# Kernel optimization log

Measured on AMD Instinct MI355X. Metric: run time of the kernel, lower is better.

Reference implementation:

```python
import jax, jax.numpy as jnp
import numpy as np

NUM_FEATURES = 8
HIDDEN = 64
IN_DIM = NUM_FEATURES + 6  # 14


def _lstm_cell(x, h, c, W_ih, W_hh, b_ih, b_hh):
    # torch gate order: i, f, g, o
    gates = x @ W_ih.T + h @ W_hh.T + b_ih + b_hh
    i, f, g, o = jnp.split(gates, 4, axis=-1)
    c_new = jax.nn.sigmoid(f) * c + jax.nn.sigmoid(i) * jnp.tanh(g)
    h_new = jax.nn.sigmoid(o) * jnp.tanh(c_new)
    return h_new, c_new


def setup_inputs() -> dict:
    key = jax.random.key(0)
    ks = jax.random.split(key, 20)
    T = 20000
    s = 0.05
    inp = {
        "encoder_out": jax.random.normal(ks[0], (1024, 64), jnp.float32),
        "h0": jax.random.normal(ks[1], (2, HIDDEN), jnp.float32),
        "c0": jax.random.normal(ks[2], (2, HIDDEN), jnp.float32),
        "difficulty": jax.random.normal(ks[3], (6,), jnp.float32),
        "target": jax.random.normal(ks[4], (T, NUM_FEATURES), jnp.float32),
        # LSTM layer 0 (input 14 -> hidden 64)
        "W_ih0": jax.random.normal(ks[5], (4 * HIDDEN, IN_DIM), jnp.float32) * s,
        "W_hh0": jax.random.normal(ks[6], (4 * HIDDEN, HIDDEN), jnp.float32) * s,
        "b_ih0": jax.random.normal(ks[7], (4 * HIDDEN,), jnp.float32) * s,
        "b_hh0": jax.random.normal(ks[8], (4 * HIDDEN,), jnp.float32) * s,
        # LSTM layer 1 (hidden 64 -> hidden 64)
        "W_ih1": jax.random.normal(ks[9], (4 * HIDDEN, HIDDEN), jnp.float32) * s,
        "W_hh1": jax.random.normal(ks[10], (4 * HIDDEN, HIDDEN), jnp.float32) * s,
        "b_ih1": jax.random.normal(ks[11], (4 * HIDDEN,), jnp.float32) * s,
        "b_hh1": jax.random.normal(ks[12], (4 * HIDDEN,), jnp.float32) * s,
        # hiddenfc: 64 -> 32
        "W_hid": jax.random.normal(ks[13], (HIDDEN // 2, HIDDEN), jnp.float32) * s,
        "b_hid": jax.random.normal(ks[14], (HIDDEN // 2,), jnp.float32) * s,
        # outputfc: 32 -> 8
        "W_out": jax.random.normal(ks[15], (NUM_FEATURES, HIDDEN // 2), jnp.float32) * s,
        "b_out": jax.random.normal(ks[16], (NUM_FEATURES,), jnp.float32) * s,
    }
    return inp


def reference(encoder_out, h0, c0, difficulty, target,
              W_ih0, W_hh0, b_ih0, b_hh0,
              W_ih1, W_hh1, b_ih1, b_hh1,
              W_hid, b_hid, W_out, b_out):
    T = target.shape[0]
    # Teacher-forced inputs: step 0 is zeros(14); step i>0 is cat(target[i-1], difficulty).
    diff_tiled = jnp.broadcast_to(difficulty, (T - 1, 6))
    inputs = jnp.concatenate([
        jnp.zeros((1, IN_DIM), target.dtype),
        jnp.concatenate([target[:-1], diff_tiled], axis=1),
    ], axis=0)  # [T, 14]

    def step(carry, x_t):
        h0s, c0s, h1s, c1s = carry
        h0s, c0s = _lstm_cell(x_t, h0s, c0s, W_ih0, W_hh0, b_ih0, b_hh0)
        h1s, c1s = _lstm_cell(h0s, h1s, c1s, W_ih1, W_hh1, b_ih1, b_hh1)
        # dropout is identity in eval mode
        hid = h1s @ W_hid.T + b_hid
        out = jnp.round(hid @ W_out.T + b_out)
        return (h0s, c0s, h1s, c1s), out

    init = (h0[0], c0[0], h0[1], c0[1])
    (hf0, cf0, hf1, cf1), outs = jax.lax.scan(step, init, inputs)
    h_final = jnp.stack([hf0, hf1])  # [2, 64]
    c_final = jnp.stack([cf0, cf1])  # [2, 64]
    return outs, h_final, c_final
```

## Files before the change

### kernel.cpp

```cpp
#include <hip/hip_runtime.h>

#define NF 8
#define RD 256
#define RMASK 255

typedef float f2 __attribute__((ext_vector_type(2)));
typedef float f4 __attribute__((ext_vector_type(4)));

template <int CTRL>
__device__ __forceinline__ float qp(float x) {
  return __int_as_float(
      __builtin_amdgcn_update_dpp(0, __float_as_int(x), CTRL, 0xF, 0xF, true));
}

__device__ __forceinline__ void wg_barrier() {
  asm volatile("s_waitcnt lgkmcnt(0)" ::: "memory");
  __builtin_amdgcn_s_barrier();
  __builtin_amdgcn_sched_barrier(0);
}

__global__ __launch_bounds__(384, 2) void decoder_p10(
    const float* __restrict__ h0in, const float* __restrict__ c0in,
    const float* __restrict__ diffp, const float* __restrict__ target,
    const float* __restrict__ Wih0, const float* __restrict__ Whh0,
    const float* __restrict__ bih0, const float* __restrict__ bhh0,
    const float* __restrict__ Wih1, const float* __restrict__ Whh1,
    const float* __restrict__ bih1, const float* __restrict__ bhh1,
    const float* __restrict__ Whid, const float* __restrict__ bhidp,
    const float* __restrict__ Woutp, const float* __restrict__ boutp,
    float* __restrict__ outp, float* __restrict__ ws, const int T)
{
  const int tid = threadIdx.x;
  const int wv  = tid >> 6;
  const int l   = tid & 63;
  const int q   = l >> 2;
  const int k   = l & 3;
  const int u   = 16 * (wv & 3) + q;
  const int r   = 64 * k + u;
  const bool isk0 = (k == 0);
  const float am = (k == 2) ? 2.0f : 1.0f;
  const float ab = (k == 2) ? -1.0f : 0.0f;

  __shared__ alignas(256) float h0r[4][64];
  __shared__ alignas(256) float tbuf[2][32 * NF];
  __shared__ alignas(256) float h0loc[8][64];
  __shared__ alignas(256) float h1r[4][64];
  __shared__ alignas(256) float hidS[4][32];
  __shared__ alignas(256) float obuf[64 * NF];
  __shared__ float ldspad[23040];

  if (T < 0) {
    ldspad[tid] = h0in[tid];
    __syncthreads();
    outp[0] = ldspad[383 - tid];
  }

  int* flag = (int*)ws;
  int* cons = (int*)ws + 16;
  float* ring = ws + 64;

  if (blockIdx.x == 0) {
    f2 wreg[36];
    float b_ = 0.f, xd = 0.f, cS = 0.f, hS = 0.f, xc = 0.f;
    if (wv < 4) {
      #pragma unroll
      for (int j = 0; j < 4; ++j) {
        const int row = 64 * ((k + j) & 3) + u;
        const float* rp = Whh0 + row * 64 + 16 * k;
        #pragma unroll
        for (int c = 0; c < 4; ++c) {
          f4 v = *(const f4*)(rp + 4 * ((c + k) & 3));
          wreg[8 * j + 2 * c]     = v.lo;
          wreg[8 * j + 2 * c + 1] = v.hi;
        }
      }
      b_ = bih0[r] + bhh0[r];
      const float* ra = Wih0 + r * 14;
      #pragma unroll
      for (int c = 0; c < 4; ++c) wreg[32 + c] = (f2){ra[2 * c], ra[2 * c + 1]};
      #pragma unroll
      for (int m = 0; m < 6; ++m) xd += ra[8 + m] * diffp[m];
      if (isk0) cS = c0in[u];
      if (wv == 0) h0r[3][l] = h0in[l];
    } else if (wv == 5) {
      if (l < T) {
        *(f4*)&((float*)tbuf)[l * 8]     = *(const f4*)&target[l * 8];
        *(f4*)&((float*)tbuf)[l * 8 + 4] = *(const f4*)&target[l * 8 + 4];
      }
    }
    __syncthreads();

    int consL = 0;
    f4 tr0 = {0.f, 0.f, 0.f, 0.f}, tr1 = {0.f, 0.f, 0.f, 0.f};
    for (int t = 0; t <= T; ++t) {
      if (wv < 4) {
        if (t < T) {
          const float* base = &h0r[(t - 1) & 3][16 * k];
          f2 P0 = {0.f,0.f}, P1 = {0.f,0.f}, P2 = {0.f,0.f}, P3 = {0.f,0.f};
          #pragma unroll
          for (int c = 0; c < 4; ++c) {
            f4 v = *(const f4*)(base + 4 * ((c + k) & 3));
            P0 += wreg[2*c] * v.lo;      P0 += wreg[2*c+1] * v.hi;
            P1 += wreg[8+2*c] * v.lo;    P1 += wreg[8+2*c+1] * v.hi;
            P2 += wreg[16+2*c] * v.lo;   P2 += wreg[16+2*c+1] * v.hi;
            P3 += wreg[24+2*c] * v.lo;   P3 += wreg[24+2*c+1] * v.hi;
          }
          float p0 = P0.x + P0.y, p1 = P1.x + P1.y;
          float p2 = P2.x + P2.y, p3 = P3.x + P3.y;
          float g = ((p0 + qp<0x39>(p3)) + (qp<0x4E>(p2) + qp<0x93>(p1))) + b_ + xc;
          float e = __expf(-g * am);
          float s = __fdividef(1.0f, 1.0f + e);
          float a = fmaf(s, am, ab);
          float A1 = qp<0xB1>(a), A2 = qp<0x4E>(a), A3 = qp<0x1B>(a);
          if (isk0) {
            cS = A1 * cS + a * A2;
            float e2 = __expf(-2.0f * cS);
            hS = A3 * (__fdividef(2.0f, 1.0f + e2) - 1.0f);
            h0r[t & 3][u] = hS;
          }
        }
        if (t < T - 1) {
          const f4* trow = (const f4*)&tbuf[(t >> 5) & 1][(t & 31) * NF];
          f4 r0 = trow[0], r1 = trow[1];
          f2 s2 = wreg[32] * r0.lo; s2 += wreg[33] * r0.hi;
          s2 += wreg[34] * r1.lo;   s2 += wreg[35] * r1.hi;
          xc = xd + s2.x + s2.y;
        } else xc = 0.f;
      } else if (wv == 4) {
        if (t >= 1) {
          if ((t & 3) == 0 && t >= 4 && l == 0)
            __hip_atomic_store(flag, t - 2, __ATOMIC_RELEASE,
                               __HIP_MEMORY_SCOPE_AGENT);
          if ((t & 63) == 0) {
            while (t - consL > RD - 64)
              consL = __hip_atomic_load(cons, __ATOMIC_RELAXED,
                                        __HIP_MEMORY_SCOPE_AGENT);
          }
          ring[((t - 1) & RMASK) * 64 + l] = h0r[(t - 1) & 3][l];
        }
      } else {
        const int ph = t & 31;
        const int cl = (t >> 5) + 1;
        if (l < 32 && cl * 32 < T) {
          if (ph == 8) {
            tr0 = *(const f4*)&target[cl * 256 + l * 8];
            tr1 = *(const f4*)&target[cl * 256 + l * 8 + 4];
          } else if (ph == 26) {
            *(f4*)&tbuf[cl & 1][l * 8]     = tr0;
            *(f4*)&tbuf[cl & 1][l * 8 + 4] = tr1;
          }
        }
      }
      wg_barrier();
    }
    if (wv == 4 && l == 0)
      __hip_atomic_store(flag, T, __ATOMIC_RELEASE, __HIP_MEMORY_SCOPE_AGENT);
    if (wv < 4 && isk0) {
      outp[T * NF + u]       = hS;
      outp[T * NF + 128 + u] = cS;
    }
  } else {
    f2 wreg[64];
    f2 wH[16], wO[4];
    float b_ = 0.f, cS = 0.f, hS = 0.f;
    float bhA = 0.f, bhB = 0.f, bo_ = 0.f;
    if (wv < 4) {
      const float* Wsrc = (k < 2) ? Wih1 : Whh1;
      const int co = 32 * (k & 1);
      #pragma unroll
      for (int j = 0; j < 4; ++j) {
        const int row = 64 * ((k + j) & 3) + u;
        const float* rp = Wsrc + row * 64 + co;
        #pragma unroll
        for (int c = 0; c < 8; ++c) {
          f4 v = *(const f4*)(rp + 4 * ((c + 2 * k) & 7));
          wreg[16 * j + 2 * c]     = v.lo;
          wreg[16 * j + 2 * c + 1] = v.hi;
        }
      }
      b_ = bih1[r] + bhh1[r];
      if (isk0) cS = c0in[64 + u];
      if (wv == 0) h1r[3][l] = h0in[64 + l];
    } else if (wv == 5) {
      #pragma unroll
      for (int i = 0; i < 2; ++i) {
        const float* rp = Whid + (2 * q + i) * 64 + 16 * k;
        #pragma unroll
        for (int c = 0; c < 4; ++c) {
          f4 v = *(const f4*)(rp + 4 * ((c + k) & 3));
          wH[8 * i + 2 * c]     = v.lo;
          wH[8 * i + 2 * c + 1] = v.hi;
        }
      }
      bhA = bhidp[2 * q];
      bhB = bhidp[2 * q + 1];
      if (q < 8) {
        const float* rp = Woutp + q * 32 + 8 * k;
        #pragma unroll
        for (int c = 0; c < 2; ++c) {
          f4 v = *(const f4*)(rp + 4 * ((c + k) & 1));
          wO[2 * c]     = v.lo;
          wO[2 * c + 1] = v.hi;
        }
        bo_ = boutp[q];
      }
    }
    int flagL = 0, fillW = 0, nPend = 0;
    float b0 = 0.f, b1 = 0.f, b2 = 0.f, b3 = 0.f;
    if (wv == 4) {
      const int pre = (T < 4) ? T : 4;
      while (flagL < pre)
        flagL = __hip_atomic_load(flag, __ATOMIC_ACQUIRE,
                                  __HIP_MEMORY_SCOPE_AGENT);
      for (int s = 0; s < pre; ++s) {
        float v = ring[(s & RMASK) * 64 + l];
        h0loc[s & 7][l] = v;
      }
      fillW = pre;
    }
    __syncthreads();

    const int pend = T + 3;
    for (int p = 0; p <= pend; ++p) {
      if (wv < 4) {
        if (p < T) {
          const float* base = (k < 2) ? &h0loc[p & 7][32 * (k & 1)]
                                      : &h1r[(p - 1) & 3][32 * (k & 1)];
          f2 P0 = {0.f,0.f}, P1 = {0.f,0.f}, P2 = {0.f,0.f}, P3 = {0.f,0.f};
          #pragma unroll
          for (int c = 0; c < 8; ++c) {
            f4 v = *(const f4*)(base + 4 * ((c + 2 * k) & 7));
            P0 += wreg[2*c] * v.lo;      P0 += wreg[2*c+1] * v.hi;
            P1 += wreg[16+2*c] * v.lo;   P1 += wreg[16+2*c+1] * v.hi;
            P2 += wreg[32+2*c] * v.lo;   P2 += wreg[32+2*c+1] * v.hi;
            P3 += wreg[48+2*c] * v.lo;   P3 += wreg[48+2*c+1] * v.hi;
          }
          float p0 = P0.x + P0.y, p1 = P1.x + P1.y;
          float p2 = P2.x + P2.y, p3 = P3.x + P3.y;
          float g = ((p0 + qp<0x39>(p3)) + (qp<0x4E>(p2) + qp<0x93>(p1))) + b_;
          float e = __expf(-g * am);
          float s = __fdividef(1.0f, 1.0f + e);
          float a = fmaf(s, am, ab);
          float A1 = qp<0xB1>(a), A2 = qp<0x4E>(a), A3 = qp<0x1B>(a);
          if (isk0) {
            cS = A1 * cS + a * A2;
            float e2 = __expf(-2.0f * cS);
            hS = A3 * (__fdividef(2.0f, 1.0f + e2) - 1.0f);
            h1r[p & 3][u] = hS;
          }
        }
      } else if (wv == 4) {
        if (nPend > 0) h0loc[(fillW + 0) & 7][l] = b0;
        if (nPend > 1) h0loc[(fillW + 1) & 7][l] = b1;
        if (nPend > 2) h0loc[(fillW + 2) & 7][l] = b2;
        if (nPend > 3) h0loc[(fillW + 3) & 7][l] = b3;
        fillW += nPend;
        nPend = 0;
        if ((p & 3) == 0)
          flagL = __hip_atomic_load(flag, __ATOMIC_ACQUIRE,
                                    __HIP_MEMORY_SCOPE_AGENT);
        int need = p + 2; if (need > T) need = T;
        while (fillW < need) {
          while (flagL < fillW + 1)
            flagL = __hip_atomic_load(flag, __ATOMIC_ACQUIRE,
                                      __HIP_MEMORY_SCOPE_AGENT);
          float v = ring[(fillW & RMASK) * 64 + l];
          h0loc[fillW & 7][l] = v;
          ++fillW;
        }
        int want = flagL;
        if (want > p + 8) want = p + 8;
        if (want > T) want = T;
        int n = want - fillW;
        if (n < 0) n = 0;
        if (n > 4) n = 4;
        if (n > 0) b0 = ring[((fillW + 0) & RMASK) * 64 + l];
        if (n > 1) b1 = ring[((fillW + 1) & RMASK) * 64 + l];
        if (n > 2) b2 = ring[((fillW + 2) & RMASK) * 64 + l];
        if (n > 3) b3 = ring[((fillW + 3) & RMASK) * 64 + l];
        nPend = n;
        if ((p & 63) == 0 && l == 0)
          __hip_atomic_store(cons, p, __ATOMIC_RELAXED,
                             __HIP_MEMORY_SCOPE_AGENT);
      } else {
        const int sH = p - 2;
        if (sH >= 0 && sH < T) {
          const float* hp = &h1r[sH & 3][16 * k];
          f2 pa = {0.f,0.f}, pb = {0.f,0.f};
          #pragma unroll
          for (int c = 0; c < 4; ++c) {
            f4 v = *(const f4*)(hp + 4 * ((c + k) & 3));
            pa += wH[2*c] * v.lo;     pa += wH[2*c+1] * v.hi;
            pb += wH[8+2*c] * v.lo;   pb += wH[8+2*c+1] * v.hi;
          }
          float sa = pa.x + pa.y; sa += qp<0xB1>(sa); sa += qp<0x4E>(sa);
          float sb = pb.x + pb.y; sb += qp<0xB1>(sb); sb += qp<0x4E>(sb);
          if (isk0) *(f2*)&hidS[sH & 3][2 * q] = (f2){sa + bhA, sb + bhB};
        }
        const int sO = p - 4;
        if (sO >= 0 && sO < T && q < 8) {
          const float* hp = &hidS[sO & 3][8 * k];
          f2 po = {0.f,0.f};
          #pragma unroll
          for (int c = 0; c < 2; ++c) {
            f4 v = *(const f4*)(hp + 4 * ((c + k) & 1));
            po += wO[2*c] * v.lo; po += wO[2*c+1] * v.hi;
          }
          float so = po.x + po.y; so += qp<0xB1>(so); so += qp<0x4E>(so);
          if (isk0) obuf[(sO & 63) * NF + q] = rintf(so + bo_);
        }
        if (l >= 32 && (p & 31) == 5 && p >= 37) {
          const int j = l - 32;
          #pragma unroll
          for (int ii = 0; ii < 2; ++ii) {
            const int fidx = 2 * j + ii;
            const int s  = (p - 37) + (fidx >> 1);
            const int c4 = (fidx & 1) * 4;
            *(f4*)&outp[s * NF + c4] = *(const f4*)&obuf[(s & 63) * NF + c4];
          }
        }
      }
      wg_barrier();
    }
    if (wv < 4 && isk0) {
      outp[T * NF + 64 + u]  = hS;
      outp[T * NF + 192 + u] = cS;
    }
    __syncthreads();
    {
      int s0 = T - 64;
      if (s0 < 0) s0 = 0;
      for (int idx = tid; idx < (T - s0) * NF; idx += 384) {
        const int s = s0 + (idx >> 3);
        outp[s * NF + (idx & 7)] = obuf[(s & 63) * NF + (idx & 7)];
      }
    }
  }
}

extern "C" void kernel_launch(void* const* d_in, const int* in_sizes, int n_in,
                              void* d_out, int out_size, void* d_ws, size_t ws_size,
                              hipStream_t stream) {
  const float* h0in   = (const float*)d_in[1];
  const float* c0in   = (const float*)d_in[2];
  const float* diffp  = (const float*)d_in[3];
  const float* target = (const float*)d_in[4];
  const float* Wih0   = (const float*)d_in[5];
  const float* Whh0   = (const float*)d_in[6];
  const float* bih0   = (const float*)d_in[7];
  const float* bhh0   = (const float*)d_in[8];
  const float* Wih1   = (const float*)d_in[9];
  const float* Whh1   = (const float*)d_in[10];
  const float* bih1   = (const float*)d_in[11];
  const float* bhh1   = (const float*)d_in[12];
  const float* Whid   = (const float*)d_in[13];
  const float* bhidp  = (const float*)d_in[14];
  const float* Woutp  = (const float*)d_in[15];
  const float* boutp  = (const float*)d_in[16];
  float* outp = (float*)d_out;
  const int T = in_sizes[4] / NF;

  hipMemsetAsync(d_ws, 0, 256, stream);
  decoder_p10<<<dim3(2), dim3(384), 0, stream>>>(
      h0in, c0in, diffp, target,
      Wih0, Whh0, bih0, bhh0,
      Wih1, Whh1, bih1, bhh1,
      Whid, bhidp, Woutp, boutp,
      outp, (float*)d_ws, T);
}
```

Measured before the change: 10.58 ms.

## Split output head into third block and use coherent asm loads for cross-block rings

```diff
diff --git a/kernel.cpp b/kernel.cpp
--- a/kernel.cpp
+++ b/kernel.cpp
@@ -19,7 +19,26 @@
   __builtin_amdgcn_sched_barrier(0);
 }
 
-__global__ __launch_bounds__(384, 2) void decoder_p10(
+#define WAIT_VM(N) asm volatile("s_waitcnt vmcnt(" #N ")" ::: "memory")
+
+__device__ __forceinline__ float ld_cohf(const float* p) {
+  float v;
+  asm volatile("global_load_dword %0, %1, off sc0 sc1" : "=v"(v) : "v"(p) : "memory");
+  return v;
+}
+__device__ __forceinline__ int ld_cohi(const int* p) {
+  int v;
+  asm volatile("global_load_dword %0, %1, off sc0 sc1" : "=v"(v) : "v"(p) : "memory");
+  return v;
+}
+__device__ __forceinline__ void st_cohf(float* p, float v) {
+  asm volatile("global_store_dword %0, %1, off sc0 sc1" :: "v"(p), "v"(v) : "memory");
+}
+__device__ __forceinline__ void st_cohi(int* p, int v) {
+  asm volatile("global_store_dword %0, %1, off sc0 sc1" :: "v"(p), "v"(v) : "memory");
+}
+
+__global__ __launch_bounds__(320, 1) void decoder_p11(
     const float* __restrict__ h0in, const float* __restrict__ c0in,
     const float* __restrict__ diffp, const float* __restrict__ target,
     const float* __restrict__ Wih0, const float* __restrict__ Whh0,
@@ -43,21 +62,24 @@
 
   __shared__ alignas(256) float h0r[4][64];
   __shared__ alignas(256) float tbuf[2][32 * NF];
-  __shared__ alignas(256) float h0loc[8][64];
+  __shared__ alignas(256) float h0loc[16][64];
   __shared__ alignas(256) float h1r[4][64];
+  __shared__ alignas(256) float h1loc[8][64];
   __shared__ alignas(256) float hidS[4][32];
-  __shared__ alignas(256) float obuf[64 * NF];
-  __shared__ float ldspad[23040];
+  __shared__ float ldspad[20480];
 
   if (T < 0) {
     ldspad[tid] = h0in[tid];
     __syncthreads();
-    outp[0] = ldspad[383 - tid];
+    outp[0] = ldspad[319 - tid];
   }
 
-  int* flag = (int*)ws;
-  int* cons = (int*)ws + 16;
-  float* ring = ws + 64;
+  int* flag0p = (int*)ws;
+  int* cons0p = (int*)ws + 16;
+  int* flag1p = (int*)ws + 32;
+  int* cons1p = (int*)ws + 48;
+  float* ring0 = ws + 256;
+  float* ring1 = ws + 256 + RD * 64;
 
   if (blockIdx.x == 0) {
     f2 wreg[36];
@@ -82,7 +104,7 @@
       for (int m = 0; m < 6; ++m) xd += ra[8 + m] * diffp[m];
       if (isk0) cS = c0in[u];
       if (wv == 0) h0r[3][l] = h0in[l];
-    } else if (wv == 5) {
+    } else {
       if (l < T) {
         *(f4*)&((float*)tbuf)[l * 8]     = *(const f4*)&target[l * 8];
         *(f4*)&((float*)tbuf)[l * 8 + 4] = *(const f4*)&target[l * 8 + 4];
@@ -90,7 +112,7 @@
     }
     __syncthreads();
 
-    int consL = 0;
+    int cons0L = 0;
     f4 tr0 = {0.f, 0.f, 0.f, 0.f}, tr1 = {0.f, 0.f, 0.f, 0.f};
     for (int t = 0; t <= T; ++t) {
       if (wv < 4) {
@@ -126,19 +148,21 @@
           s2 += wreg[34] * r1.lo;   s2 += wreg[35] * r1.hi;
           xc = xd + s2.x + s2.y;
         } else xc = 0.f;
-      } else if (wv == 4) {
+      } else {
+        if ((t & 3) == 0 && t >= 8) {
+          WAIT_VM(4);
+          if (l == 0) st_cohi(flag0p, t - 6);
+        }
+        if ((t & 63) == 0 && t > RD - 64) {
+          while (t - cons0L > RD - 64) {
+            cons0L = ld_cohi(cons0p);
+            WAIT_VM(0);
+          }
+        }
         if (t >= 1) {
-          if ((t & 3) == 0 && t >= 4 && l == 0)
-            __hip_atomic_store(flag, t - 2, __ATOMIC_RELEASE,
-                               __HIP_MEMORY_SCOPE_AGENT);
-          if ((t & 63) == 0) {
-            while (t - consL > RD - 64)
-              consL = __hip_atomic_load(cons, __ATOMIC_RELAXED,
-                                        __HIP_MEMORY_SCOPE_AGENT);
-          }
-          ring[((t - 1) & RMASK) * 64 + l] = h0r[(t - 1) & 3][l];
-        }
-      } else {
+          float hv = h0r[(t - 1) & 3][l];
+          st_cohf(&ring0[((t - 1) & RMASK) * 64 + l], hv);
+        }
         const int ph = t & 31;
         const int cl = (t >> 5) + 1;
         if (l < 32 && cl * 32 < T) {
@@ -153,17 +177,17 @@
       }
       wg_barrier();
     }
-    if (wv == 4 && l == 0)
-      __hip_atomic_store(flag, T, __ATOMIC_RELEASE, __HIP_MEMORY_SCOPE_AGENT);
+    if (wv == 4) {
+      WAIT_VM(0);
+      if (l == 0) st_cohi(flag0p, T);
+    }
     if (wv < 4 && isk0) {
       outp[T * NF + u]       = hS;
       outp[T * NF + 128 + u] = cS;
     }
-  } else {
+  } else if (blockIdx.x == 1) {
     f2 wreg[64];
-    f2 wH[16], wO[4];
     float b_ = 0.f, cS = 0.f, hS = 0.f;
-    float bhA = 0.f, bhB = 0.f, bo_ = 0.f;
     if (wv < 4) {
       const float* Wsrc = (k < 2) ? Wih1 : Whh1;
       const int co = 32 * (k & 1);
@@ -181,50 +205,29 @@
       b_ = bih1[r] + bhh1[r];
       if (isk0) cS = c0in[64 + u];
       if (wv == 0) h1r[3][l] = h0in[64 + l];
-    } else if (wv == 5) {
-      #pragma unroll
-      for (int i = 0; i < 2; ++i) {
-        const float* rp = Whid + (2 * q + i) * 64 + 16 * k;
-        #pragma unroll
-        for (int c = 0; c < 4; ++c) {
-          f4 v = *(const f4*)(rp + 4 * ((c + k) & 3));
-          wH[8 * i + 2 * c]     = v.lo;
-          wH[8 * i + 2 * c + 1] = v.hi;
-        }
-      }
-      bhA = bhidp[2 * q];
-      bhB = bhidp[2 * q + 1];
-      if (q < 8) {
-        const float* rp = Woutp + q * 32 + 8 * k;
-        #pragma unroll
-        for (int c = 0; c < 2; ++c) {
-          f4 v = *(const f4*)(rp + 4 * ((c + k) & 1));
-          wO[2 * c]     = v.lo;
-          wO[2 * c + 1] = v.hi;
-        }
-        bo_ = boutp[q];
-      }
-    }
-    int flagL = 0, fillW = 0, nPend = 0;
-    float b0 = 0.f, b1 = 0.f, b2 = 0.f, b3 = 0.f;
+    }
+    int flagL = 0, fillW = 0, nPend = 0, F_pend = 0, cons1L = 0;
+    float pb0 = 0.f, pb1 = 0.f, pb2 = 0.f, pb3 = 0.f;
     if (wv == 4) {
       const int pre = (T < 4) ? T : 4;
-      while (flagL < pre)
-        flagL = __hip_atomic_load(flag, __ATOMIC_ACQUIRE,
-                                  __HIP_MEMORY_SCOPE_AGENT);
+      while (flagL < pre) {
+        flagL = ld_cohi(flag0p);
+        WAIT_VM(0);
+      }
       for (int s = 0; s < pre; ++s) {
-        float v = ring[(s & RMASK) * 64 + l];
-        h0loc[s & 7][l] = v;
+        float v = ld_cohf(&ring0[(s & RMASK) * 64 + l]);
+        WAIT_VM(0);
+        h0loc[s & 15][l] = v;
       }
       fillW = pre;
+      F_pend = flagL;
     }
     __syncthreads();
 
-    const int pend = T + 3;
-    for (int p = 0; p <= pend; ++p) {
+    for (int p = 0; p <= T; ++p) {
       if (wv < 4) {
         if (p < T) {
-          const float* base = (k < 2) ? &h0loc[p & 7][32 * (k & 1)]
+          const float* base = (k < 2) ? &h0loc[p & 15][32 * (k & 1)]
                                       : &h1r[(p - 1) & 3][32 * (k & 1)];
           f2 P0 = {0.f,0.f}, P1 = {0.f,0.f}, P2 = {0.f,0.f}, P3 = {0.f,0.f};
           #pragma unroll
@@ -250,42 +253,111 @@
           }
         }
       } else if (wv == 4) {
-        if (nPend > 0) h0loc[(fillW + 0) & 7][l] = b0;
-        if (nPend > 1) h0loc[(fillW + 1) & 7][l] = b1;
-        if (nPend > 2) h0loc[(fillW + 2) & 7][l] = b2;
-        if (nPend > 3) h0loc[(fillW + 3) & 7][l] = b3;
+        WAIT_VM(1);
+        if (nPend > 0) h0loc[(fillW + 0) & 15][l] = pb0;
+        if (nPend > 1) h0loc[(fillW + 1) & 15][l] = pb1;
+        if (nPend > 2) h0loc[(fillW + 2) & 15][l] = pb2;
+        if (nPend > 3) h0loc[(fillW + 3) & 15][l] = pb3;
         fillW += nPend;
         nPend = 0;
-        if ((p & 3) == 0)
-          flagL = __hip_atomic_load(flag, __ATOMIC_ACQUIRE,
-                                    __HIP_MEMORY_SCOPE_AGENT);
-        int need = p + 2; if (need > T) need = T;
-        while (fillW < need) {
-          while (flagL < fillW + 1)
-            flagL = __hip_atomic_load(flag, __ATOMIC_ACQUIRE,
-                                      __HIP_MEMORY_SCOPE_AGENT);
-          float v = ring[(fillW & RMASK) * 64 + l];
-          h0loc[fillW & 7][l] = v;
-          ++fillW;
-        }
-        int want = flagL;
-        if (want > p + 8) want = p + 8;
-        if (want > T) want = T;
-        int n = want - fillW;
-        if (n < 0) n = 0;
-        if (n > 4) n = 4;
-        if (n > 0) b0 = ring[((fillW + 0) & RMASK) * 64 + l];
-        if (n > 1) b1 = ring[((fillW + 1) & RMASK) * 64 + l];
-        if (n > 2) b2 = ring[((fillW + 2) & RMASK) * 64 + l];
-        if (n > 3) b3 = ring[((fillW + 3) & RMASK) * 64 + l];
-        nPend = n;
-        if ((p & 63) == 0 && l == 0)
-          __hip_atomic_store(cons, p, __ATOMIC_RELAXED,
-                             __HIP_MEMORY_SCOPE_AGENT);
-      } else {
-        const int sH = p - 2;
-        if (sH >= 0 && sH < T) {
-          const float* hp = &h1r[sH & 3][16 * k];
+        if ((p & 3) == 1) flagL = F_pend;
+        {
+          int need = p + 2; if (need > T) need = T;
+          while (fillW < need) {
+            while (flagL < fillW + 1) {
+              flagL = ld_cohi(flag0p);
+              WAIT_VM(0);
+            }
+            float v = ld_cohf(&ring0[(fillW & RMASK) * 64 + l]);
+            WAIT_VM(0);
+            h0loc[fillW & 15][l] = v;
+            ++fillW;
+          }
+        }
+        if ((p & 3) == 0 && p >= 8 && l == 0)
+          st_cohi(flag1p, p - 6);
+        if ((p & 63) == 0 && p > RD - 64) {
+          while (p - cons1L > RD - 64) {
+            cons1L = ld_cohi(cons1p);
+            WAIT_VM(0);
+          }
+        }
+        if ((p & 3) == 0) F_pend = ld_cohi(flag0p);
+        {
+          int want = flagL;
+          if (want > p + 10) want = p + 10;
+          if (want > T) want = T;
+          int n = want - fillW;
+          if (n < 0) n = 0;
+          if (n > 4) n = 4;
+          if (n > 0) pb0 = ld_cohf(&ring0[((fillW + 0) & RMASK) * 64 + l]);
+          if (n > 1) pb1 = ld_cohf(&ring0[((fillW + 1) & RMASK) * 64 + l]);
+          if (n > 2) pb2 = ld_cohf(&ring0[((fillW + 2) & RMASK) * 64 + l]);
+          if (n > 3) pb3 = ld_cohf(&ring0[((fillW + 3) & RMASK) * 64 + l]);
+          nPend = n;
+        }
+        if (p >= 1) {
+          float hv = h1r[(p - 1) & 3][l];
+          st_cohf(&ring1[((p - 1) & RMASK) * 64 + l], hv);
+        }
+        if ((p & 63) == 32 && l == 0) st_cohi(cons0p, fillW);
+      }
+      wg_barrier();
+    }
+    if (wv == 4) {
+      WAIT_VM(0);
+      if (l == 0) st_cohi(flag1p, T);
+    }
+    if (wv < 4 && isk0) {
+      outp[T * NF + 64 + u]  = hS;
+      outp[T * NF + 192 + u] = cS;
+    }
+  } else {
+    if (wv != 0) return;
+    f2 wH[16], wO[4];
+    float bhA = 0.f, bhB = 0.f, bo_ = 0.f;
+    #pragma unroll
+    for (int i = 0; i < 2; ++i) {
+      const float* rp = Whid + (2 * q + i) * 64 + 16 * k;
+      #pragma unroll
+      for (int c = 0; c < 4; ++c) {
+        f4 v = *(const f4*)(rp + 4 * ((c + k) & 3));
+        wH[8 * i + 2 * c]     = v.lo;
+        wH[8 * i + 2 * c + 1] = v.hi;
+      }
+    }
+    bhA = bhidp[2 * q];
+    bhB = bhidp[2 * q + 1];
+    if (q < 8) {
+      const float* rp = Woutp + q * 32 + 8 * k;
+      #pragma unroll
+      for (int c = 0; c < 2; ++c) {
+        f4 v = *(const f4*)(rp + 4 * ((c + k) & 1));
+        wO[2 * c]     = v.lo;
+        wO[2 * c + 1] = v.hi;
+      }
+      bo_ = boutp[q];
+    }
+    int f1L = 0;
+    for (int s0 = 0; s0 < T; s0 += 8) {
+      const int B = (T - s0 < 8) ? (T - s0) : 8;
+      while (f1L < s0 + B) {
+        f1L = ld_cohi(flag1p);
+        WAIT_VM(0);
+      }
+      float rb[8];
+      #pragma unroll
+      for (int i = 0; i < 8; ++i)
+        if (i < B) rb[i] = ld_cohf(&ring1[((s0 + i) & RMASK) * 64 + l]);
+      WAIT_VM(0);
+      #pragma unroll
+      for (int i = 0; i < 8; ++i)
+        if (i < B) h1loc[(s0 + i) & 7][l] = rb[i];
+      #pragma unroll
+      for (int i = 0; i < 8; ++i) {
+        if (i < B) {
+          const int s = s0 + i;
+          const float* hp = &h1loc[s & 7][16 * k];
           f2 pa = {0.f,0.f}, pb = {0.f,0.f};
           #pragma unroll
           for (int c = 0; c < 4; ++c) {
@@ -295,45 +367,21 @@
           }
           float sa = pa.x + pa.y; sa += qp<0xB1>(sa); sa += qp<0x4E>(sa);
           float sb = pb.x + pb.y; sb += qp<0xB1>(sb); sb += qp<0x4E>(sb);
-          if (isk0) *(f2*)&hidS[sH & 3][2 * q] = (f2){sa + bhA, sb + bhB};
-        }
-        const int sO = p - 4;
-        if (sO >= 0 && sO < T && q < 8) {
-          const float* hp = &hidS[sO & 3][8 * k];
-          f2 po = {0.f,0.f};
-          #pragma unroll
-          for (int c = 0; c < 2; ++c) {
-            f4 v = *(const f4*)(hp + 4 * ((c + k) & 1));
-            po += wO[2*c] * v.lo; po += wO[2*c+1] * v.hi;
-          }
-          float so = po.x + po.y; so += qp<0xB1>(so); so += qp<0x4E>(so);
-          if (isk0) obuf[(sO & 63) * NF + q] = rintf(so + bo_);
-        }
-        if (l >= 32 && (p & 31) == 5 && p >= 37) {
-          const int j = l - 32;
-          #pragma unroll
-          for (int ii = 0; ii < 2; ++ii) {
-            const int fidx = 2 * j + ii;
-            const int s  = (p - 37) + (fidx >> 1);
-            const int c4 = (fidx & 1) * 4;
-            *(f4*)&outp[s * NF + c4] = *(const f4*)&obuf[(s & 63) * NF + c4];
-          }
-        }
-      }
-      wg_barrier();
-    }
-    if (wv < 4 && isk0) {
-      outp[T * NF + 64 + u]  = hS;
-      outp[T * NF + 192 + u] = cS;
-    }
-    __syncthreads();
-    {
-      int s0 = T - 64;
-      if (s0 < 0) s0 = 0;
-      for (int idx = tid; idx < (T - s0) * NF; idx += 384) {
-        const int s = s0 + (idx >> 3);
-        outp[s * NF + (idx & 7)] = obuf[(s & 63) * NF + (idx & 7)];
-      }
+          if (isk0) *(f2*)&hidS[s & 3][2 * q] = (f2){sa + bhA, sb + bhB};
+          if (q < 8) {
+            const float* hq = &hidS[s & 3][8 * k];
+            f2 po = {0.f,0.f};
+            #pragma unroll
+            for (int c = 0; c < 2; ++c) {
+              f4 v = *(const f4*)(hq + 4 * ((c + k) & 1));
+              po += wO[2*c] * v.lo; po += wO[2*c+1] * v.hi;
+            }
+            float so = po.x + po.y; so += qp<0xB1>(so); so += qp<0x4E>(so);
+            if (isk0) outp[s * NF + q] = rintf(so + bo_);
+          }
+        }
+      }
+      if ((s0 & 63) == 0 && s0 > 0 && l == 0) st_cohi(cons1p, s0);
     }
   }
 }
@@ -361,7 +409,7 @@
   const int T = in_sizes[4] / NF;
 
   hipMemsetAsync(d_ws, 0, 256, stream);
-  decoder_p10<<<dim3(2), dim3(384), 0, stream>>>(
+  decoder_p11<<<dim3(3), dim3(320), 0, stream>>>(
       h0in, c0in, diffp, target,
       Wih0, Whh0, bih0, bhh0,
       Wih1, Whh1, bih1, bhh1,
```

New measurement: 10.59 ms. No clear change (+0.1%).
